# Performance work log

Hardware: AMD Instinct MI355X
Metric: run time of the kernel (lower is better)

The kernel has to match this reference:

```python
import jax, jax.numpy as jnp
import numpy as np

NUM_EMBEDDINGS = 4096
EMBEDDING_DIM = 256
COMMITMENT_COST = 0.25
DECAY = 0.99
EPS = 1e-5
NORM_EPS = 1e-6
B, T = 64, 1024


def _l2norm(x):
    # torch.nn.functional.normalize: x / max(||x||_2, eps)
    n = jnp.sqrt(jnp.sum(x * x, axis=-1, keepdims=True))
    return x / jnp.maximum(n, NORM_EPS)


def setup_inputs() -> dict:
    key = jax.random.key(0)
    k1, k2 = jax.random.split(key)
    z = jax.random.normal(k1, (B, EMBEDDING_DIM, T), dtype=jnp.float32)
    weight = jax.random.normal(k2, (NUM_EMBEDDINGS, EMBEDDING_DIM), dtype=jnp.float32)
    weight = weight.at[0].set(0.0)  # reserved zero code
    ema_cluster_size = jnp.zeros((NUM_EMBEDDINGS,), dtype=jnp.float32)
    ema_w = weight  # buffer initialized as a clone of the codebook
    return {"z": z, "weight": weight, "ema_cluster_size": ema_cluster_size, "ema_w": ema_w}


def reference(z, weight, ema_cluster_size, ema_w):
    K = weight.shape[0]
    zp = jnp.transpose(z, (0, 2, 1))            # [B, T, D]
    b, t, d = zp.shape
    flat_z = zp.reshape(-1, d)                  # [N, D]
    flat_z_norm = _l2norm(flat_z)
    weight_norm = _l2norm(weight)
    # cosine similarity; argmin(1 - cos) == argmax(cos); code 0 excluded via -inf
    cos_sim = jnp.einsum('nd,kd->nk', flat_z_norm, weight_norm)
    cos_sim = cos_sim.at[:, 0].set(-jnp.inf)
    idx = jnp.argmax(cos_sim, axis=1)           # [N] int
    q = weight[idx].reshape(zp.shape)           # [B, T, D]

    # --- training-mode EMA codebook update (buffer math, no grad) ---
    counts = jax.ops.segment_sum(jnp.ones_like(idx, dtype=flat_z.dtype), idx, num_segments=K)
    new_cs = DECAY * ema_cluster_size + (1.0 - DECAY) * counts
    dw = jax.ops.segment_sum(flat_z_norm, idx, num_segments=K)  # [K, D]
    new_ema_w = DECAY * ema_w + (1.0 - DECAY) * dw
    new_cs = new_cs.at[0].set(0.0)
    new_ema_w = new_ema_w.at[0].set(0.0)
    n = jnp.sum(new_cs)
    cluster_size = (new_cs + EPS) / (n + K * EPS) * n
    new_weight = _l2norm(new_ema_w / cluster_size[:, None])
    new_weight = new_weight.at[0].set(0.0)

    loss = COMMITMENT_COST * jnp.mean((jax.lax.stop_gradient(q) - zp) ** 2)
    quantized = zp + jax.lax.stop_gradient(q - zp)  # straight-through
    quantized = jnp.transpose(quantized, (0, 2, 1))  # back to [B, D, T]
    codes = idx.reshape(b, t)
    return quantized, loss, codes, new_weight, new_cs, new_ema_w
```

## Files before the change

kernel.cpp:

```cpp
#include <hip/hip_runtime.h>
#include <math.h>

#define NUM_K 4096
#define DIM   256
#define TLEN  1024
#define DT    (DIM * TLEN)
#define WCAP  1024

typedef short bf16x8 __attribute__((ext_vector_type(8)));
typedef float f32x4  __attribute__((ext_vector_type(4)));

static __device__ __forceinline__ unsigned short f2bf(float x) {
  unsigned u = __float_as_uint(x);
  u += 0x7fffu + ((u >> 16) & 1u);
  return (unsigned short)(u >> 16);
}

static __device__ __forceinline__ f32x4 mfma16(bf16x8 a, bf16x8 b, f32x4 c) {
  return __builtin_amdgcn_mfma_f32_16x16x32_bf16(a, b, c, 0, 0, 0);
}

static __device__ __forceinline__ float dppmax16(float v) {
  int x = __float_as_int(v); int y;
  y = __builtin_amdgcn_update_dpp(x, x, 0xB1, 0xF, 0xF, false);
  v = fmaxf(v, __int_as_float(y)); x = __float_as_int(v);
  y = __builtin_amdgcn_update_dpp(x, x, 0x4E, 0xF, 0xF, false);
  v = fmaxf(v, __int_as_float(y)); x = __float_as_int(v);
  y = __builtin_amdgcn_update_dpp(x, x, 0x141, 0xF, 0xF, false);
  v = fmaxf(v, __int_as_float(y)); x = __float_as_int(v);
  y = __builtin_amdgcn_update_dpp(x, x, 0x140, 0xF, 0xF, false);
  v = fmaxf(v, __int_as_float(y));
  return v;
}

__global__ __launch_bounds__(256) void wnorm_kernel(const float* __restrict__ w,
                                                    float* __restrict__ wnorms) {
  const int k = blockIdx.x * 256 + threadIdx.x;
  const float* row = w + (size_t)k * DIM;
  float p[2];
#pragma unroll
  for (int blk = 0; blk < 2; ++blk) {
    const float* b = row + blk * 128;
    float r[8];
#pragma unroll
    for (int j = 0; j < 8; ++j) r[j] = __fmul_rn(b[j], b[j]);
    for (int i = 8; i < 128; i += 8) {
#pragma unroll
      for (int j = 0; j < 8; ++j) r[j] = __fadd_rn(r[j], __fmul_rn(b[i + j], b[i + j]));
    }
    p[blk] = __fadd_rn(__fadd_rn(__fadd_rn(r[0], r[1]), __fadd_rn(r[2], r[3])),
                       __fadd_rn(__fadd_rn(r[4], r[5]), __fadd_rn(r[6], r[7])));
  }
  wnorms[k] = fmaxf(__fsqrt_rn(__fadd_rn(p[0], p[1])), 1e-6f);
}

__global__ __launch_bounds__(256) void wnf32_kernel(const float* __restrict__ w,
                                                    const float* __restrict__ wnorms,
                                                    float* __restrict__ wnf) {
  const int idx = blockIdx.x * 256 + threadIdx.x;
  const float m = wnorms[idx >> 6];
  const float4 v = *reinterpret_cast<const float4*>(w + (size_t)idx * 4);
  float4 o;
  o.x = __fdiv_rn(v.x, m); o.y = __fdiv_rn(v.y, m);
  o.z = __fdiv_rn(v.z, m); o.w = __fdiv_rn(v.w, m);
  *reinterpret_cast<float4*>(wnf + (size_t)idx * 4) = o;
}

__global__ __launch_bounds__(256) void wfrag_kernel(const float* __restrict__ wnf,
                                                    unsigned short* __restrict__ img) {
  const int t = blockIdx.x * 256 + threadIdx.x;
  const int lane = t & 63;
  const int fragid = t >> 6;
  const int jg = fragid & 3;
  const int kb = (fragid >> 2) & 7;
  const int chunk = fragid >> 5;
  const int c  = (chunk << 6) + (jg << 4) + (lane & 15);
  const int d0 = (kb << 5) + ((lane >> 4) << 3);
  const float* src = wnf + (size_t)c * DIM + d0;
  union { bf16x8 v; unsigned short u[8]; } o;
#pragma unroll
  for (int u = 0; u < 8; ++u) o.u[u] = f2bf(src[u]);
  *reinterpret_cast<bf16x8*>(img + (size_t)fragid * 512 + lane * 8) = o.v;
}

__global__ __launch_bounds__(256, 2) void vq_main_kernel(
    const float* __restrict__ z, const float* __restrict__ weight,
    const unsigned short* __restrict__ wimg, const float* __restrict__ wnf32,
    float* __restrict__ znT, float* __restrict__ out_codes,
    float* __restrict__ counts, float* __restrict__ loss_accum) {
  __shared__ float pp[2][64];
  __shared__ float tnorm[64];
  __shared__ int   fidx[64];
  __shared__ int   clist[4][WCAP];
  __shared__ int   wcnt[4];
  __shared__ unsigned long long tokbest[64];

  const int tid  = threadIdx.x;
  const int bb   = blockIdx.x >> 4;
  const int t0   = (blockIdx.x & 15) << 6;
  const int lane = tid & 63;
  const int wv   = tid >> 6;
  const int wr   = wv >> 1;
  const int wc   = wv & 1;
  const float* zb = z + (size_t)bb * DT + t0;

  if (tid < 128) {
    const int tok = tid & 63, blk = tid >> 6;
    const float* zc = zb + tok;
    float r[8];
#pragma unroll
    for (int j = 0; j < 8; ++j) {
      const float v = zc[(size_t)(blk * 128 + j) * TLEN];
      r[j] = __fmul_rn(v, v);
    }
    for (int i = 8; i < 128; i += 8) {
#pragma unroll
      for (int j = 0; j < 8; ++j) {
        const float v = zc[(size_t)(blk * 128 + i + j) * TLEN];
        r[j] = __fadd_rn(r[j], __fmul_rn(v, v));
      }
    }
    pp[blk][tok] = __fadd_rn(__fadd_rn(__fadd_rn(r[0], r[1]), __fadd_rn(r[2], r[3])),
                             __fadd_rn(__fadd_rn(r[4], r[5]), __fadd_rn(r[6], r[7])));
  }
  if (tid < 4)  wcnt[tid] = 0;
  if (tid < 64) tokbest[tid] = 0ull;
  __syncthreads();
  if (tid < 64) tnorm[tid] = fmaxf(__fsqrt_rn(__fadd_rn(pp[0][tid], pp[1][tid])), 1e-6f);
  __syncthreads();

  {
    const int tok = tid & 63, seg = tid >> 6;
    const float m = tnorm[tok];
    const float* zc = zb + tok;
    float* orow = znT + (size_t)((bb << 10) + t0 + tok) * DIM + (seg << 6);
#pragma unroll 4
    for (int k4 = 0; k4 < 16; ++k4) {
      float4 o;
      o.x = __fdiv_rn(zc[(size_t)((seg << 6) + (k4 << 2) + 0) * TLEN], m);
      o.y = __fdiv_rn(zc[(size_t)((seg << 6) + (k4 << 2) + 1) * TLEN], m);
      o.z = __fdiv_rn(zc[(size_t)((seg << 6) + (k4 << 2) + 2) * TLEN], m);
      o.w = __fdiv_rn(zc[(size_t)((seg << 6) + (k4 << 2) + 3) * TLEN], m);
      *reinterpret_cast<float4*>(&orow[k4 << 2]) = o;
    }
  }

  bf16x8 afr[2][8];
  {
    const int tloc = (wr << 5) + (lane & 15);
    const int dr   = (lane >> 4) << 3;
#pragma unroll
    for (int i = 0; i < 2; ++i) {
      const float* zc = zb + tloc + (i << 4);
#pragma unroll
      for (int kb = 0; kb < 8; ++kb) {
        union { bf16x8 v; unsigned short u[8]; } a;
#pragma unroll
        for (int u = 0; u < 8; ++u)
          a.u[u] = f2bf(zc[(size_t)((kb << 5) + dr + u) * TLEN]);
        afr[i][kb] = a.v;
      }
    }
  }

  float wloc[2][4];
  {
    const int tb = (wr << 5) + ((lane >> 4) << 2);
#pragma unroll
    for (int i = 0; i < 2; ++i)
#pragma unroll
      for (int r = 0; r < 4; ++r) wloc[i][r] = 0.02f * tnorm[tb + (i << 4) + r];
  }

  const unsigned short* bbase = wimg + (wc << 10) + (lane << 3);
  const f32x4 zero4 = {0.f, 0.f, 0.f, 0.f};
  const bool lc0 = (wc == 0) && ((lane & 15) == 0);

#define LOADC(buf, ch) do {                                              \
    const unsigned short* p_ = bbase + ((size_t)(ch) << 14);             \
    _Pragma("unroll")                                                    \
    for (int kb_ = 0; kb_ < 8; ++kb_) {                                  \
      buf[kb_]     = *reinterpret_cast<const bf16x8*>(p_ + (kb_ << 11)); \
      buf[kb_ + 8] = *reinterpret_cast<const bf16x8*>(p_ + (kb_ << 11) + 512); \
    }                                                                    \
    __builtin_amdgcn_sched_barrier(0);                                   \
  } while (0)

#define MFMAC(buf, accv) do {                                            \
    __builtin_amdgcn_s_setprio(1);                                       \
    _Pragma("unroll")                                                    \
    for (int kb_ = 0; kb_ < 8; ++kb_) {                                  \
      accv[0][0] = mfma16(afr[0][kb_], buf[kb_],     accv[0][0]);        \
      accv[1][0] = mfma16(afr[1][kb_], buf[kb_],     accv[1][0]);        \
      accv[0][1] = mfma16(afr[0][kb_], buf[kb_ + 8], accv[0][1]);        \
      accv[1][1] = mfma16(afr[1][kb_], buf[kb_ + 8], accv[1][1]);        \
    }                                                                    \
    __builtin_amdgcn_s_setprio(0);                                       \
  } while (0)

#define PROCESS(accv, ch) do {                                           \
    if ((ch) == 0 && lc0) {                                              \
      _Pragma("unroll") for (int i_ = 0; i_ < 2; ++i_)                   \
      _Pragma("unroll") for (int r_ = 0; r_ < 4; ++r_)                   \
        accv[i_][0][r_] = -INFINITY;                                     \
    }                                                                    \
    _Pragma("unroll")                                                    \
    for (int i_ = 0; i_ < 2; ++i_) {                                     \
      _Pragma("unroll")                                                  \
      for (int r_ = 0; r_ < 4; ++r_) {                                   \
        float m_ = fmaxf(accv[i_][0][r_], accv[i_][1][r_]);              \
        m_ = dppmax16(m_);                                               \
        v1loc[i_][r_] = fmaxf(v1loc[i_][r_], m_);                        \
        const float t_ = v1loc[i_][r_] - wloc[i_][r_];                   \
        _Pragma("unroll")                                                \
        for (int j_ = 0; j_ < 2; ++j_) {                                 \
          if (accv[i_][j_][r_] >= t_) {                                  \
            const int c_ = ((ch) << 6) + (wc << 5) + (j_ << 4) + (lane & 15); \
            if (c_ != 0) {                                               \
              const int pos_ = atomicAdd(&wcnt[wv], 1);                  \
              if (pos_ < WCAP)                                           \
                clist[wv][pos_] = (c_ << 6) | ((wr << 5) + (i_ << 4) + ((lane >> 4) << 2) + r_); \
            }                                                            \
          }                                                              \
        }                                                                \
      }                                                                  \
    }                                                                    \
  } while (0)

  float v1loc[2][4];
#pragma unroll
  for (int i = 0; i < 2; ++i)
#pragma unroll
    for (int r = 0; r < 4; ++r) v1loc[i][r] = -INFINITY;
  {
    bf16x8 bA[16], bB[16];
    LOADC(bA, 0);
#pragma unroll 1
    for (int chunk = 0; chunk < 64; chunk += 2) {
      LOADC(bB, chunk + 1);
      f32x4 acc[2][2];
      acc[0][0] = zero4; acc[0][1] = zero4; acc[1][0] = zero4; acc[1][1] = zero4;
      MFMAC(bA, acc);
      PROCESS(acc, chunk);
      if (chunk + 2 < 64) LOADC(bA, chunk + 2);
      f32x4 ac2[2][2];
      ac2[0][0] = zero4; ac2[0][1] = zero4; ac2[1][0] = zero4; ac2[1][1] = zero4;
      MFMAC(bB, ac2);
      PROCESS(ac2, chunk + 1);
    }
  }
#undef LOADC
#undef MFMAC
#undef PROCESS
  __syncthreads();

#pragma unroll 1
  for (int w = 0; w < 4; ++w) {
    const int n = min(wcnt[w], WCAP);
    for (int e = tid; e < n; e += 256) {
      const int pk = clist[w][e];
      const int tloc = pk & 63;
      const int c = pk >> 6;
      const float* za = znT + (size_t)((bb << 10) + t0 + tloc) * DIM;
      const float* wa = wnf32 + (size_t)c * DIM;
      float s = 0.f;
#pragma unroll 8
      for (int d = 0; d < DIM; ++d)
        s = fmaf(za[d], wa[d], s);
      unsigned uk = __float_as_uint(s);
      uk = (uk & 0x80000000u) ? ~uk : (uk | 0x80000000u);
      const unsigned long long key =
          ((unsigned long long)uk << 32) | (unsigned)(4095 - c);
      atomicMax(&tokbest[tloc], key);
    }
  }
  __syncthreads();

  if (tid < 64) {
    const unsigned long long key = tokbest[tid];
    const int bc = 4095 - (int)(key & 0xFFFull);
    fidx[tid] = bc;
    out_codes[bb * TLEN + t0 + tid] = (float)bc;
    atomicAdd(&counts[bc], 1.0f);
  }
  __syncthreads();

  {
    float lpart = 0.f;
#pragma unroll 4
    for (int r = 0; r < 16; ++r) {
      const int tk = (r << 2) + wv;
      const int code = fidx[tk];
      const float* zc = zb + tk;
      const float4 w4 = *reinterpret_cast<const float4*>(
          weight + (size_t)code * DIM + (lane << 2));
      float4 zr4;
      zr4.x = zc[(size_t)((lane << 2) + 0) * TLEN];
      zr4.y = zc[(size_t)((lane << 2) + 1) * TLEN];
      zr4.z = zc[(size_t)((lane << 2) + 2) * TLEN];
      zr4.w = zc[(size_t)((lane << 2) + 3) * TLEN];
      const float dx = w4.x - zr4.x, dy = w4.y - zr4.y;
      const float dz = w4.z - zr4.z, dw_ = w4.w - zr4.w;
      lpart = fmaf(dx, dx, lpart); lpart = fmaf(dy, dy, lpart);
      lpart = fmaf(dz, dz, lpart); lpart = fmaf(dw_, dw_, lpart);
    }
#pragma unroll
    for (int off = 32; off; off >>= 1) lpart += __shfl_down(lpart, off, 64);
    if (lane == 0) atomicAdd(loss_accum, lpart);
  }
}

__global__ __launch_bounds__(256) void finalize_cs_kernel(
    const float* __restrict__ counts, const float* __restrict__ ema_cs,
    float* __restrict__ out_ncs, float* __restrict__ ws_n,
    const float* __restrict__ loss_accum, float* __restrict__ out_loss,
    int* __restrict__ offsets) {
  __shared__ float redf[4];
  __shared__ int   redi[4];
  const int tid = threadIdx.x;
  const int lane = tid & 63, wv = tid >> 6;
  const int base = tid << 4;
  int cloc[16]; int csum = 0; float fsum = 0.f;
#pragma unroll
  for (int j = 0; j < 16; ++j) {
    const int k = base + j;
    const float cf = counts[k];
    const float v = (k == 0) ? 0.f : 0.99f * ema_cs[k] + 0.01f * cf;
    out_ncs[k] = v; fsum += v;
    cloc[j] = csum; csum += (int)cf;
  }
  int inc = csum;
#pragma unroll
  for (int off = 1; off < 64; off <<= 1) {
    const int t = __shfl_up(inc, off, 64);
    if (lane >= off) inc += t;
  }
  float fs = fsum;
#pragma unroll
  for (int off = 32; off; off >>= 1) fs += __shfl_down(fs, off, 64);
  if (lane == 63) redi[wv] = inc;
  if (lane == 0)  redf[wv] = fs;
  __syncthreads();
  int wbase = 0;
#pragma unroll
  for (int w = 0; w < 4; ++w) wbase += (w < wv) ? redi[w] : 0;
  const int tbase = wbase + inc - csum;
#pragma unroll
  for (int j = 0; j < 16; ++j) offsets[base + j] = tbase + cloc[j];
  if (tid == 0) {
    ws_n[0] = redf[0] + redf[1] + redf[2] + redf[3];
    out_loss[0] = 0.25f * loss_accum[0] / 16777216.0f;
  }
}

__global__ __launch_bounds__(256) void scatter_kernel(
    const float* __restrict__ codes, const int* __restrict__ offsets,
    int* __restrict__ cursor, int* __restrict__ bucket) {
  const int g = blockIdx.x * 256 + threadIdx.x;
  const int c = (int)codes[g];
  const int pos = atomicAdd(&cursor[c], 1);
  bucket[offsets[c] + pos] = g;
}

__global__ __launch_bounds__(256) void dw_kernel(
    const float* __restrict__ znT, const float* __restrict__ counts,
    const int* __restrict__ offsets, const int* __restrict__ bucket,
    float* __restrict__ dw) {
  const int c = blockIdx.x;
  const int cnt = (int)counts[c];
  const int off = offsets[c];
  const int tid = threadIdx.x;
  float acc = 0.f;
  for (int i = 0; i < cnt; ++i) {
    const int g = bucket[off + i];
    acc += znT[(size_t)g * DIM + tid];
  }
  dw[(size_t)c * DIM + tid] = acc;
}

__global__ __launch_bounds__(256) void finalize_w_kernel(
    const float* __restrict__ ema_w, const float* __restrict__ ncs,
    const float* __restrict__ ws_n, float* __restrict__ new_ema_w,
    float* __restrict__ new_weight) {
  const int wid  = threadIdx.x >> 6;
  const int lane = threadIdx.x & 63;
  const int k    = (blockIdx.x << 2) + wid;
  const float n  = ws_n[0];
  const float cs = (ncs[k] + 1e-5f) / (n + 4096.0f * 1e-5f) * n;
  const float* erow = ema_w + k * DIM;
  float* nrow = new_ema_w + k * DIM;
  float* wrow = new_weight + k * DIM;
  const int d0 = lane << 2;
  float u[4]; float ss = 0.f;
#pragma unroll
  for (int j = 0; j < 4; ++j) {
    const float dwv = nrow[d0 + j];
    const float val = (k == 0) ? 0.f : 0.99f * erow[d0 + j] + 0.01f * dwv;
    nrow[d0 + j] = val;
    const float uu = val / cs;
    u[j] = uu;
    ss = fmaf(uu, uu, ss);
  }
#pragma unroll
  for (int off = 32; off; off >>= 1) ss += __shfl_xor(ss, off, 64);
  const float m = fmaxf(sqrtf(ss), 1e-6f);
#pragma unroll
  for (int j = 0; j < 4; ++j) wrow[d0 + j] = u[j] / m;
}

__global__ __launch_bounds__(256) void qwrite_kernel(
    const float* __restrict__ codes, const float* __restrict__ weight,
    float* __restrict__ out_q) {
  const int bb = blockIdx.x >> 4;
  const int t0 = (blockIdx.x & 15) << 6;
  const int ln = threadIdx.x & 63, qv = threadIdx.x >> 6;
  const int code = (int)codes[bb * TLEN + t0 + ln];
  const float* wrow = weight + (size_t)code * DIM;
  float* qb = out_q + (size_t)bb * DT + t0 + ln;
#pragma unroll 4
  for (int dd = 0; dd < 64; ++dd) {
    const int d = (qv << 6) + dd;
    qb[(size_t)d * TLEN] = wrow[d];
  }
}

extern "C" void kernel_launch(void* const* d_in, const int* in_sizes, int n_in,
                              void* d_out, int out_size, void* d_ws, size_t ws_size,
                              hipStream_t stream) {
  const float* z      = (const float*)d_in[0];
  const float* weight = (const float*)d_in[1];
  const float* ema_cs = (const float*)d_in[2];
  const float* ema_w  = (const float*)d_in[3];

  float* out = (float*)d_out;
  float* out_q     = out;
  float* out_loss  = out + 16777216;
  float* out_codes = out + 16777217;
  float* out_nw    = out + 16842753;
  float* out_ncs   = out + 17891329;
  float* out_new   = out + 17895425;

  float* counts     = (float*)d_ws;
  float* loss_accum = counts + 4096;
  float* ws_n       = counts + 4097;
  float* wnorms     = counts + 4352;

  unsigned short* wimg = (unsigned short*)(out_nw + 3);
  int* bucket  = (int*)(out_nw + 3);
  int* offsets = (int*)(out_nw + 524292);
  int* cursor  = (int*)(out_nw + 528388);
  float* wnf32 = out_new;

  hipMemsetAsync(d_ws, 0, 4098 * sizeof(float), stream);
  hipMemsetAsync(cursor, 0, 4096 * sizeof(int), stream);

  wnorm_kernel<<<16, 256, 0, stream>>>(weight, wnorms);
  wnf32_kernel<<<1024, 256, 0, stream>>>(weight, wnorms, wnf32);
  wfrag_kernel<<<512, 256, 0, stream>>>(wnf32, wimg);
  vq_main_kernel<<<1024, 256, 0, stream>>>(z, weight, wimg, wnf32, out_q ,
                                           out_codes, counts, loss_accum);
  finalize_cs_kernel<<<1, 256, 0, stream>>>(counts, ema_cs, out_ncs, ws_n,
                                            loss_accum, out_loss, offsets);
  scatter_kernel<<<256, 256, 0, stream>>>(out_codes, offsets, cursor, bucket);
  dw_kernel<<<NUM_K, 256, 0, stream>>>(out_q , counts, offsets, bucket, out_new);
  finalize_w_kernel<<<NUM_K / 4, 256, 0, stream>>>(ema_w, out_ncs, ws_n,
                                                   out_new, out_nw);
  qwrite_kernel<<<1024, 256, 0, stream>>>(out_codes, weight, out_q);
}
```

Measured before the change: 896.0 us.

## Deepen codebook prefetch with manual vmcnt waits and pool candidate list

Codebook fragment loads now use inline-asm global_load_dwordx4 with explicit s_waitcnt vmcnt(16), so two chunks stay in flight and the next chunk's load is issued right after its buffer's MFMAs finish. The aim is to hide global-memory latency behind the MFMA and candidate-filter work. The four per-wave candidate lists become one shared list with a single shared counter, and the rescoring loop handles two candidates per thread per iteration to spread the work evenly and give more memory-level parallelism. The risks are more contention on the single shared atomic counter, and the fragile inline-asm wait counts, which depend on exactly how many loads the compiler has outstanding.

```diff
diff --git a/kernel.cpp b/kernel.cpp
--- a/kernel.cpp
+++ b/kernel.cpp
@@ -5,7 +5,7 @@
 #define DIM   256
 #define TLEN  1024
 #define DT    (DIM * TLEN)
-#define WCAP  1024
+#define CAP   4096
 
 typedef short bf16x8 __attribute__((ext_vector_type(8)));
 typedef float f32x4  __attribute__((ext_vector_type(4)));
@@ -91,8 +91,8 @@
   __shared__ float pp[2][64];
   __shared__ float tnorm[64];
   __shared__ int   fidx[64];
-  __shared__ int   clist[4][WCAP];
-  __shared__ int   wcnt[4];
+  __shared__ int   clist[CAP];
+  __shared__ int   ccount;
   __shared__ unsigned long long tokbest[64];
 
   const int tid  = threadIdx.x;
@@ -123,8 +123,8 @@
     pp[blk][tok] = __fadd_rn(__fadd_rn(__fadd_rn(r[0], r[1]), __fadd_rn(r[2], r[3])),
                              __fadd_rn(__fadd_rn(r[4], r[5]), __fadd_rn(r[6], r[7])));
   }
-  if (tid < 4)  wcnt[tid] = 0;
-  if (tid < 64) tokbest[tid] = 0ull;
+  if (tid == 0)  ccount = 0;
+  if (tid < 64)  tokbest[tid] = 0ull;
   __syncthreads();
   if (tid < 64) tnorm[tid] = fmaxf(__fsqrt_rn(__fadd_rn(pp[0][tid], pp[1][tid])), 1e-6f);
   __syncthreads();
@@ -172,28 +172,37 @@
       for (int r = 0; r < 4; ++r) wloc[i][r] = 0.02f * tnorm[tb + (i << 4) + r];
   }
 
-  const unsigned short* bbase = wimg + (wc << 10) + (lane << 3);
+  const char* bbase = (const char*)wimg + (wc << 11) + (lane << 4);
   const f32x4 zero4 = {0.f, 0.f, 0.f, 0.f};
   const bool lc0 = (wc == 0) && ((lane & 15) == 0);
 
+#define GLOAD(dst, ptr) \
+  asm volatile("global_load_dwordx4 %0, %1, off" : "=v"(dst) : "v"(ptr))
+
 #define LOADC(buf, ch) do {                                              \
-    const unsigned short* p_ = bbase + ((size_t)(ch) << 14);             \
+    const char* pc_ = bbase + ((size_t)(ch) << 15);                      \
     _Pragma("unroll")                                                    \
     for (int kb_ = 0; kb_ < 8; ++kb_) {                                  \
-      buf[kb_]     = *reinterpret_cast<const bf16x8*>(p_ + (kb_ << 11)); \
-      buf[kb_ + 8] = *reinterpret_cast<const bf16x8*>(p_ + (kb_ << 11) + 512); \
+      GLOAD(buf[kb_],     pc_ + (kb_ << 12));                            \
+      GLOAD(buf[kb_ + 8], pc_ + (kb_ << 12) + 1024);                     \
     }                                                                    \
-    __builtin_amdgcn_sched_barrier(0);                                   \
   } while (0)
+
+#define VMWAIT16() do { asm volatile("s_waitcnt vmcnt(16)" ::: "memory"); \
+                        __builtin_amdgcn_sched_barrier(0); } while (0)
+#define VMWAIT0()  do { asm volatile("s_waitcnt vmcnt(0)"  ::: "memory"); \
+                        __builtin_amdgcn_sched_barrier(0); } while (0)
 
 #define MFMAC(buf, accv) do {                                            \
     __builtin_amdgcn_s_setprio(1);                                       \
     _Pragma("unroll")                                                    \
     for (int kb_ = 0; kb_ < 8; ++kb_) {                                  \
-      accv[0][0] = mfma16(afr[0][kb_], buf[kb_],     accv[0][0]);        \
-      accv[1][0] = mfma16(afr[1][kb_], buf[kb_],     accv[1][0]);        \
-      accv[0][1] = mfma16(afr[0][kb_], buf[kb_ + 8], accv[0][1]);        \
-      accv[1][1] = mfma16(afr[1][kb_], buf[kb_ + 8], accv[1][1]);        \
+      const bf16x8 b0_ = __builtin_bit_cast(bf16x8, buf[kb_]);           \
+      const bf16x8 b1_ = __builtin_bit_cast(bf16x8, buf[kb_ + 8]);       \
+      accv[0][0] = mfma16(afr[0][kb_], b0_, accv[0][0]);                 \
+      accv[1][0] = mfma16(afr[1][kb_], b0_, accv[1][0]);                 \
+      accv[0][1] = mfma16(afr[0][kb_], b1_, accv[0][1]);                 \
+      accv[1][1] = mfma16(afr[1][kb_], b1_, accv[1][1]);                 \
     }                                                                    \
     __builtin_amdgcn_s_setprio(0);                                       \
   } while (0)
@@ -217,9 +226,9 @@
           if (accv[i_][j_][r_] >= t_) {                                  \
             const int c_ = ((ch) << 6) + (wc << 5) + (j_ << 4) + (lane & 15); \
             if (c_ != 0) {                                               \
-              const int pos_ = atomicAdd(&wcnt[wv], 1);                  \
-              if (pos_ < WCAP)                                           \
-                clist[wv][pos_] = (c_ << 6) | ((wr << 5) + (i_ << 4) + ((lane >> 4) << 2) + r_); \
+              const int pos_ = atomicAdd(&ccount, 1);                    \
+              if (pos_ < CAP)                                            \
+                clist[pos_] = (c_ << 6) | ((wr << 5) + (i_ << 4) + ((lane >> 4) << 2) + r_); \
             }                                                            \
           }                                                              \
         }                                                                \
@@ -233,45 +242,69 @@
 #pragma unroll
     for (int r = 0; r < 4; ++r) v1loc[i][r] = -INFINITY;
   {
-    bf16x8 bA[16], bB[16];
+    asm volatile("s_waitcnt vmcnt(0)" ::: "memory");
+    f32x4 bA[16], bB[16];
     LOADC(bA, 0);
+    LOADC(bB, 1);
 #pragma unroll 1
-    for (int chunk = 0; chunk < 64; chunk += 2) {
-      LOADC(bB, chunk + 1);
+    for (int chunk = 0; chunk < 62; chunk += 2) {
+      VMWAIT16();
       f32x4 acc[2][2];
       acc[0][0] = zero4; acc[0][1] = zero4; acc[1][0] = zero4; acc[1][1] = zero4;
       MFMAC(bA, acc);
+      LOADC(bA, chunk + 2);
       PROCESS(acc, chunk);
-      if (chunk + 2 < 64) LOADC(bA, chunk + 2);
+      VMWAIT16();
       f32x4 ac2[2][2];
       ac2[0][0] = zero4; ac2[0][1] = zero4; ac2[1][0] = zero4; ac2[1][1] = zero4;
       MFMAC(bB, ac2);
+      LOADC(bB, chunk + 3);
       PROCESS(ac2, chunk + 1);
     }
-  }
+    VMWAIT16();
+    f32x4 acc[2][2];
+    acc[0][0] = zero4; acc[0][1] = zero4; acc[1][0] = zero4; acc[1][1] = zero4;
+    MFMAC(bA, acc);
+    PROCESS(acc, 62);
+    VMWAIT0();
+    f32x4 ac2[2][2];
+    ac2[0][0] = zero4; ac2[0][1] = zero4; ac2[1][0] = zero4; ac2[1][1] = zero4;
+    MFMAC(bB, ac2);
+    PROCESS(ac2, 63);
+  }
+#undef GLOAD
 #undef LOADC
+#undef VMWAIT16
+#undef VMWAIT0
 #undef MFMAC
 #undef PROCESS
   __syncthreads();
 
-#pragma unroll 1
-  for (int w = 0; w < 4; ++w) {
-    const int n = min(wcnt[w], WCAP);
-    for (int e = tid; e < n; e += 256) {
-      const int pk = clist[w][e];
-      const int tloc = pk & 63;
-      const int c = pk >> 6;
-      const float* za = znT + (size_t)((bb << 10) + t0 + tloc) * DIM;
-      const float* wa = wnf32 + (size_t)c * DIM;
-      float s = 0.f;
+  const int ncand = min(ccount, CAP);
+  for (int e = tid; e < ncand; e += 512) {
+    const int e1v = e + 256;
+    const bool has1 = e1v < ncand;
+    const int pk0 = clist[e];
+    const int pk1 = has1 ? clist[e1v] : pk0;
+    const float* za0 = znT + (size_t)((bb << 10) + t0 + (pk0 & 63)) * DIM;
+    const float* wa0 = wnf32 + (size_t)(pk0 >> 6) * DIM;
+    const float* za1 = znT + (size_t)((bb << 10) + t0 + (pk1 & 63)) * DIM;
+    const float* wa1 = wnf32 + (size_t)(pk1 >> 6) * DIM;
+    float s0 = 0.f, s1 = 0.f;
 #pragma unroll 8
-      for (int d = 0; d < DIM; ++d)
-        s = fmaf(za[d], wa[d], s);
-      unsigned uk = __float_as_uint(s);
-      uk = (uk & 0x80000000u) ? ~uk : (uk | 0x80000000u);
-      const unsigned long long key =
-          ((unsigned long long)uk << 32) | (unsigned)(4095 - c);
-      atomicMax(&tokbest[tloc], key);
+    for (int d = 0; d < DIM; ++d) {
+      s0 = fmaf(za0[d], wa0[d], s0);
+      s1 = fmaf(za1[d], wa1[d], s1);
+    }
+    unsigned uk0 = __float_as_uint(s0);
+    uk0 = (uk0 & 0x80000000u) ? ~uk0 : (uk0 | 0x80000000u);
+    atomicMax(&tokbest[pk0 & 63],
+              ((unsigned long long)uk0 << 32) | (unsigned)(4095 - (pk0 >> 6)));
+    if (has1) {
+      unsigned uk1 = __float_as_uint(s1);
+      uk1 = (uk1 & 0x80000000u) ? ~uk1 : (uk1 | 0x80000000u);
+      atomicMax(&tokbest[pk1 & 63],
+                ((unsigned long long)uk1 << 32) | (unsigned)(4095 - (pk1 >> 6)));
     }
   }
   __syncthreads();
```

Measured after the change: 932.3 us. 4.0% more time.

## Stage codebook fragments through LDS and double token tile per block

Applied to the files above, without the earlier changes.

The main VQ kernel now uses 512-thread blocks covering 128 tokens, so each staged codebook chunk is reused by twice as many token rows. Codebook fragments are copied into a double-buffered LDS stage with direct global-to-LDS loads instead of being read into registers by each wave. The first step runs the last chunk up front to seed the running max, so early candidates are filtered against a tighter threshold. Candidates go into one shared list with a larger capacity. The dw accumulation loop is also unrolled by four to expose more independent loads. In exchange the kernel adds a block-wide barrier on every half-chunk step and uses more LDS per block, which may limit occupancy.

```diff
diff --git a/kernel.cpp b/kernel.cpp
--- a/kernel.cpp
+++ b/kernel.cpp
@@ -5,7 +5,7 @@
 #define DIM   256
 #define TLEN  1024
 #define DT    (DIM * TLEN)
-#define WCAP  1024
+#define CAP   4096
 
 typedef short bf16x8 __attribute__((ext_vector_type(8)));
 typedef float f32x4  __attribute__((ext_vector_type(4)));
@@ -18,6 +18,12 @@
 
 static __device__ __forceinline__ f32x4 mfma16(bf16x8 a, bf16x8 b, f32x4 c) {
   return __builtin_amdgcn_mfma_f32_16x16x32_bf16(a, b, c, 0, 0, 0);
+}
+
+static __device__ __forceinline__ void gl_lds16(const void* g, void* l) {
+  __builtin_amdgcn_global_load_lds(
+      (const __attribute__((address_space(1))) unsigned int*)g,
+      (__attribute__((address_space(3))) unsigned int*)l, 16, 0, 0);
 }
 
 static __device__ __forceinline__ float dppmax16(float v) {
@@ -83,57 +89,58 @@
   *reinterpret_cast<bf16x8*>(img + (size_t)fragid * 512 + lane * 8) = o.v;
 }
 
-__global__ __launch_bounds__(256, 2) void vq_main_kernel(
+__global__ __launch_bounds__(512, 4) void vq_main_kernel(
     const float* __restrict__ z, const float* __restrict__ weight,
     const unsigned short* __restrict__ wimg, const float* __restrict__ wnf32,
     float* __restrict__ znT, float* __restrict__ out_codes,
     float* __restrict__ counts, float* __restrict__ loss_accum) {
-  __shared__ float pp[2][64];
-  __shared__ float tnorm[64];
-  __shared__ int   fidx[64];
-  __shared__ int   clist[4][WCAP];
-  __shared__ int   wcnt[4];
-  __shared__ unsigned long long tokbest[64];
+  __shared__ __attribute__((aligned(16))) char bstage[2][16384];
+  __shared__ float pp[2][128];
+  __shared__ float tnorm[128];
+  __shared__ int   fidx[128];
+  __shared__ int   clist[CAP];
+  __shared__ int   ccount;
+  __shared__ unsigned long long tokbest[128];
 
   const int tid  = threadIdx.x;
-  const int bb   = blockIdx.x >> 4;
-  const int t0   = (blockIdx.x & 15) << 6;
   const int lane = tid & 63;
   const int wv   = tid >> 6;
   const int wr   = wv >> 1;
   const int wc   = wv & 1;
-  const float* zb = z + (size_t)bb * DT + t0;
-
-  if (tid < 128) {
-    const int tok = tid & 63, blk = tid >> 6;
+  const int blk  = blockIdx.x;
+  const float* zb = z + (size_t)(blk >> 3) * DT + ((blk & 7) << 7);
+  const int gtok0 = blk << 7;
+
+  if (tid < 256) {
+    const int tok = tid & 127, b2 = tid >> 7;
     const float* zc = zb + tok;
     float r[8];
 #pragma unroll
     for (int j = 0; j < 8; ++j) {
-      const float v = zc[(size_t)(blk * 128 + j) * TLEN];
+      const float v = zc[(size_t)(b2 * 128 + j) * TLEN];
       r[j] = __fmul_rn(v, v);
     }
     for (int i = 8; i < 128; i += 8) {
 #pragma unroll
       for (int j = 0; j < 8; ++j) {
-        const float v = zc[(size_t)(blk * 128 + i + j) * TLEN];
+        const float v = zc[(size_t)(b2 * 128 + i + j) * TLEN];
         r[j] = __fadd_rn(r[j], __fmul_rn(v, v));
       }
     }
-    pp[blk][tok] = __fadd_rn(__fadd_rn(__fadd_rn(r[0], r[1]), __fadd_rn(r[2], r[3])),
-                             __fadd_rn(__fadd_rn(r[4], r[5]), __fadd_rn(r[6], r[7])));
-  }
-  if (tid < 4)  wcnt[tid] = 0;
-  if (tid < 64) tokbest[tid] = 0ull;
-  __syncthreads();
-  if (tid < 64) tnorm[tid] = fmaxf(__fsqrt_rn(__fadd_rn(pp[0][tid], pp[1][tid])), 1e-6f);
+    pp[b2][tok] = __fadd_rn(__fadd_rn(__fadd_rn(r[0], r[1]), __fadd_rn(r[2], r[3])),
+                            __fadd_rn(__fadd_rn(r[4], r[5]), __fadd_rn(r[6], r[7])));
+  }
+  if (tid == 0)   ccount = 0;
+  if (tid < 128)  tokbest[tid] = 0ull;
+  __syncthreads();
+  if (tid < 128) tnorm[tid] = fmaxf(__fsqrt_rn(__fadd_rn(pp[0][tid], pp[1][tid])), 1e-6f);
   __syncthreads();
 
   {
-    const int tok = tid & 63, seg = tid >> 6;
+    const int tok = tid & 127, seg = tid >> 7;
     const float m = tnorm[tok];
     const float* zc = zb + tok;
-    float* orow = znT + (size_t)((bb << 10) + t0 + tok) * DIM + (seg << 6);
+    float* orow = znT + (size_t)(gtok0 + tok) * DIM + (seg << 6);
 #pragma unroll 4
     for (int k4 = 0; k4 < 16; ++k4) {
       float4 o;
@@ -172,115 +179,120 @@
       for (int r = 0; r < 4; ++r) wloc[i][r] = 0.02f * tnorm[tb + (i << 4) + r];
   }
 
-  const unsigned short* bbase = wimg + (wc << 10) + (lane << 3);
-  const f32x4 zero4 = {0.f, 0.f, 0.f, 0.f};
   const bool lc0 = (wc == 0) && ((lane & 15) == 0);
 
-#define LOADC(buf, ch) do {                                              \
-    const unsigned short* p_ = bbase + ((size_t)(ch) << 14);             \
-    _Pragma("unroll")                                                    \
-    for (int kb_ = 0; kb_ < 8; ++kb_) {                                  \
-      buf[kb_]     = *reinterpret_cast<const bf16x8*>(p_ + (kb_ << 11)); \
-      buf[kb_ + 8] = *reinterpret_cast<const bf16x8*>(p_ + (kb_ << 11) + 512); \
-    }                                                                    \
-    __builtin_amdgcn_sched_barrier(0);                                   \
+#define STAGE(bufi, ph) do {                                                   \
+    const char* gs_ = (const char*)wimg + ((size_t)(ph) << 14) + (wv << 10) + (lane << 4); \
+    char* ls_ = &bstage[bufi][wv << 10];                                       \
+    gl_lds16(gs_, ls_);                                                        \
+    gl_lds16(gs_ + 8192, ls_ + 8192);                                          \
   } while (0)
 
-#define MFMAC(buf, accv) do {                                            \
-    __builtin_amdgcn_s_setprio(1);                                       \
-    _Pragma("unroll")                                                    \
-    for (int kb_ = 0; kb_ < 8; ++kb_) {                                  \
-      accv[0][0] = mfma16(afr[0][kb_], buf[kb_],     accv[0][0]);        \
-      accv[1][0] = mfma16(afr[1][kb_], buf[kb_],     accv[1][0]);        \
-      accv[0][1] = mfma16(afr[0][kb_], buf[kb_ + 8], accv[0][1]);        \
-      accv[1][1] = mfma16(afr[1][kb_], buf[kb_ + 8], accv[1][1]);        \
-    }                                                                    \
-    __builtin_amdgcn_s_setprio(0);                                       \
+#define CHALF(bufi, hh) do {                                                   \
+    const char* lb_ = &bstage[bufi][(wc << 11) + (lane << 4)];                 \
+    _Pragma("unroll")                                                          \
+    for (int kb_ = 0; kb_ < 4; ++kb_) {                                        \
+      const bf16x8 b0_ = *reinterpret_cast<const bf16x8*>(lb_ + (kb_ << 12));  \
+      const bf16x8 b1_ = *reinterpret_cast<const bf16x8*>(lb_ + (kb_ << 12) + 1024); \
+      const int kg_ = ((hh) << 2) + kb_;                                       \
+      acc[0][0] = mfma16(afr[0][kg_], b0_, acc[0][0]);                         \
+      acc[1][0] = mfma16(afr[1][kg_], b0_, acc[1][0]);                         \
+      acc[0][1] = mfma16(afr[0][kg_], b1_, acc[0][1]);                         \
+      acc[1][1] = mfma16(afr[1][kg_], b1_, acc[1][1]);                         \
+    }                                                                          \
   } while (0)
 
-#define PROCESS(accv, ch) do {                                           \
-    if ((ch) == 0 && lc0) {                                              \
-      _Pragma("unroll") for (int i_ = 0; i_ < 2; ++i_)                   \
-      _Pragma("unroll") for (int r_ = 0; r_ < 4; ++r_)                   \
-        accv[i_][0][r_] = -INFINITY;                                     \
-    }                                                                    \
-    _Pragma("unroll")                                                    \
-    for (int i_ = 0; i_ < 2; ++i_) {                                     \
-      _Pragma("unroll")                                                  \
-      for (int r_ = 0; r_ < 4; ++r_) {                                   \
-        float m_ = fmaxf(accv[i_][0][r_], accv[i_][1][r_]);              \
-        m_ = dppmax16(m_);                                               \
-        v1loc[i_][r_] = fmaxf(v1loc[i_][r_], m_);                        \
-        const float t_ = v1loc[i_][r_] - wloc[i_][r_];                   \
-        _Pragma("unroll")                                                \
-        for (int j_ = 0; j_ < 2; ++j_) {                                 \
-          if (accv[i_][j_][r_] >= t_) {                                  \
-            const int c_ = ((ch) << 6) + (wc << 5) + (j_ << 4) + (lane & 15); \
-            if (c_ != 0) {                                               \
-              const int pos_ = atomicAdd(&wcnt[wv], 1);                  \
-              if (pos_ < WCAP)                                           \
-                clist[wv][pos_] = (c_ << 6) | ((wr << 5) + (i_ << 4) + ((lane >> 4) << 2) + r_); \
-            }                                                            \
-          }                                                              \
-        }                                                                \
-      }                                                                  \
-    }                                                                    \
+#define ZEROACC() do {                                                         \
+    _Pragma("unroll") for (int i_ = 0; i_ < 2; ++i_)                           \
+    _Pragma("unroll") for (int j_ = 0; j_ < 2; ++j_)                           \
+      acc[i_][j_] = (f32x4){0.f, 0.f, 0.f, 0.f};                               \
   } while (0)
 
+#define PROCESS(ch, DOC) do {                                                  \
+    if ((ch) == 0 && lc0) {                                                    \
+      _Pragma("unroll") for (int i_ = 0; i_ < 2; ++i_)                         \
+      _Pragma("unroll") for (int r_ = 0; r_ < 4; ++r_)                         \
+        acc[i_][0][r_] = -INFINITY;                                            \
+    }                                                                          \
+    _Pragma("unroll")                                                          \
+    for (int i_ = 0; i_ < 2; ++i_) {                                           \
+      _Pragma("unroll")                                                        \
+      for (int r_ = 0; r_ < 4; ++r_) {                                         \
+        float m_ = fmaxf(acc[i_][0][r_], acc[i_][1][r_]);                      \
+        m_ = dppmax16(m_);                                                     \
+        v1loc[i_][r_] = fmaxf(v1loc[i_][r_], m_);                              \
+        if (DOC) {                                                             \
+          const float t_ = v1loc[i_][r_] - wloc[i_][r_];                       \
+          _Pragma("unroll")                                                    \
+          for (int j_ = 0; j_ < 2; ++j_) {                                     \
+            if (acc[i_][j_][r_] >= t_) {                                       \
+              const int c_ = ((ch) << 6) + (wc << 5) + (j_ << 4) + (lane & 15); \
+              if (c_ != 0) {                                                   \
+                const int pos_ = atomicAdd(&ccount, 1);                        \
+                if (pos_ < CAP)                                                \
+                  clist[pos_] = (c_ << 7) | ((wr << 5) + (i_ << 4) + ((lane >> 4) << 2) + r_); \
+              }                                                                \
+            }                                                                  \
+          }                                                                    \
+        }                                                                      \
+      }                                                                        \
+    }                                                                          \
+  } while (0)
+
   float v1loc[2][4];
 #pragma unroll
   for (int i = 0; i < 2; ++i)
 #pragma unroll
     for (int r = 0; r < 4; ++r) v1loc[i][r] = -INFINITY;
-  {
-    bf16x8 bA[16], bB[16];
-    LOADC(bA, 0);
+  f32x4 acc[2][2];
+
+  STAGE(0, 126);
+  STAGE(1, 127);
+  __syncthreads();
+  ZEROACC();
+  CHALF(0, 0);
+  CHALF(1, 1);
+  PROCESS(63, 0);
+  __syncthreads();
+  STAGE(0, 0);
+
 #pragma unroll 1
-    for (int chunk = 0; chunk < 64; chunk += 2) {
-      LOADC(bB, chunk + 1);
-      f32x4 acc[2][2];
-      acc[0][0] = zero4; acc[0][1] = zero4; acc[1][0] = zero4; acc[1][1] = zero4;
-      MFMAC(bA, acc);
-      PROCESS(acc, chunk);
-      if (chunk + 2 < 64) LOADC(bA, chunk + 2);
-      f32x4 ac2[2][2];
-      ac2[0][0] = zero4; ac2[0][1] = zero4; ac2[1][0] = zero4; ac2[1][1] = zero4;
-      MFMAC(bB, ac2);
-      PROCESS(ac2, chunk + 1);
-    }
-  }
-#undef LOADC
-#undef MFMAC
+  for (int p = 0; p < 128; ++p) {
+    __syncthreads();
+    if (p + 1 < 128) STAGE((p + 1) & 1, p + 1);
+    if ((p & 1) == 0) ZEROACC();
+    CHALF(p & 1, p & 1);
+    if (p & 1) PROCESS(p >> 1, 1);
+  }
+#undef STAGE
+#undef CHALF
+#undef ZEROACC
 #undef PROCESS
   __syncthreads();
 
-#pragma unroll 1
-  for (int w = 0; w < 4; ++w) {
-    const int n = min(wcnt[w], WCAP);
-    for (int e = tid; e < n; e += 256) {
-      const int pk = clist[w][e];
-      const int tloc = pk & 63;
-      const int c = pk >> 6;
-      const float* za = znT + (size_t)((bb << 10) + t0 + tloc) * DIM;
-      const float* wa = wnf32 + (size_t)c * DIM;
-      float s = 0.f;
+  const int ncand = min(ccount, CAP);
+  for (int e = tid; e < ncand; e += 512) {
+    const int pk = clist[e];
+    const int tloc = pk & 127;
+    const int c = pk >> 7;
+    const float* za = znT + (size_t)(gtok0 + tloc) * DIM;
+    const float* wa = wnf32 + (size_t)c * DIM;
+    float s = 0.f;
 #pragma unroll 8
-      for (int d = 0; d < DIM; ++d)
-        s = fmaf(za[d], wa[d], s);
-      unsigned uk = __float_as_uint(s);
-      uk = (uk & 0x80000000u) ? ~uk : (uk | 0x80000000u);
-      const unsigned long long key =
-          ((unsigned long long)uk << 32) | (unsigned)(4095 - c);
-      atomicMax(&tokbest[tloc], key);
-    }
-  }
-  __syncthreads();
-
-  if (tid < 64) {
+    for (int d = 0; d < DIM; ++d)
+      s = fmaf(za[d], wa[d], s);
+    unsigned uk = __float_as_uint(s);
+    uk = (uk & 0x80000000u) ? ~uk : (uk | 0x80000000u);
+    atomicMax(&tokbest[tloc],
+              ((unsigned long long)uk << 32) | (unsigned)(4095 - c));
+  }
+  __syncthreads();
+
+  if (tid < 128) {
     const unsigned long long key = tokbest[tid];
     const int bc = 4095 - (int)(key & 0xFFFull);
     fidx[tid] = bc;
-    out_codes[bb * TLEN + t0 + tid] = (float)bc;
+    out_codes[gtok0 + tid] = (float)bc;
     atomicAdd(&counts[bc], 1.0f);
   }
   __syncthreads();
@@ -289,7 +301,7 @@
     float lpart = 0.f;
 #pragma unroll 4
     for (int r = 0; r < 16; ++r) {
-      const int tk = (r << 2) + wv;
+      const int tk = (r << 3) + wv;
       const int code = fidx[tk];
       const float* zc = zb + tk;
       const float4 w4 = *reinterpret_cast<const float4*>(
@@ -371,10 +383,20 @@
   const int off = offsets[c];
   const int tid = threadIdx.x;
   float acc = 0.f;
-  for (int i = 0; i < cnt; ++i) {
-    const int g = bucket[off + i];
-    acc += znT[(size_t)g * DIM + tid];
-  }
+  int i = 0;
+  for (; i + 4 <= cnt; i += 4) {
+    const int g0 = bucket[off + i + 0];
+    const int g1 = bucket[off + i + 1];
+    const int g2 = bucket[off + i + 2];
+    const int g3 = bucket[off + i + 3];
+    const float a0 = znT[(size_t)g0 * DIM + tid];
+    const float a1 = znT[(size_t)g1 * DIM + tid];
+    const float a2 = znT[(size_t)g2 * DIM + tid];
+    const float a3 = znT[(size_t)g3 * DIM + tid];
+    acc += a0 + a1 + a2 + a3;
+  }
+  for (; i < cnt; ++i)
+    acc += znT[(size_t)bucket[off + i] * DIM + tid];
   dw[(size_t)c * DIM + tid] = acc;
 }
 
@@ -457,8 +479,8 @@
   wnorm_kernel<<<16, 256, 0, stream>>>(weight, wnorms);
   wnf32_kernel<<<1024, 256, 0, stream>>>(weight, wnorms, wnf32);
   wfrag_kernel<<<512, 256, 0, stream>>>(wnf32, wimg);
-  vq_main_kernel<<<1024, 256, 0, stream>>>(z, weight, wimg, wnf32, out_q ,
-                                           out_codes, counts, loss_accum);
+  vq_main_kernel<<<512, 512, 0, stream>>>(z, weight, wimg, wnf32, out_q ,
+                                          out_codes, counts, loss_accum);
   finalize_cs_kernel<<<1, 256, 0, stream>>>(counts, ema_cs, out_ncs, ws_n,
                                             loss_accum, out_loss, offsets);
   scatter_kernel<<<256, 256, 0, stream>>>(out_codes, offsets, cursor, bucket);
```

Result: slower. 1.271 ms (+41.8%).
